# Optimization experiments

Measured on AMD Instinct MI355X. Metric: run time of the kernel, lower is better.

## Reference

```python
import jax, jax.numpy as jnp
import numpy as np

B, S, D, H = 2, 2048, 1024, 16
DK = D // H


def setup_inputs() -> dict:
    key = jax.random.key(0)
    ks = jax.random.split(key, 12)
    sc = 0.02
    inp = {
        'query': jax.random.normal(ks[0], (B, S, D), jnp.float32),
        'key': jax.random.normal(ks[1], (B, S, D), jnp.float32),
        'value': jax.random.normal(ks[2], (B, S, D), jnp.float32),
        # causal mask: positions with mask==0 are disallowed (matches masked_fill(mask==0, -inf))
        'mask': jnp.broadcast_to(jnp.tril(jnp.ones((S, S), jnp.int32)), (B, S, S)),
        'Wq': jax.random.normal(ks[3], (D, D), jnp.float32) * sc,
        'bq': jax.random.normal(ks[4], (D,), jnp.float32) * sc,
        'Wk': jax.random.normal(ks[5], (D, D), jnp.float32) * sc,
        'bk': jax.random.normal(ks[6], (D,), jnp.float32) * sc,
        'Wv': jax.random.normal(ks[7], (D, D), jnp.float32) * sc,
        'bv': jax.random.normal(ks[8], (D,), jnp.float32) * sc,
        'Wo': jax.random.normal(ks[9], (D, D), jnp.float32) * sc,
        'bo': jax.random.normal(ks[10], (D,), jnp.float32) * sc,
    }
    return inp


def reference(query, key, value, mask, Wq, bq, Wk, bk, Wv, bv, Wo, bo):
    # Linear projections (torch Linear: x @ W.T + b), split heads -> [B,H,S,DK]
    def proj(x, W, b):
        return (x @ W.T + b).reshape(B, S, H, DK).transpose(0, 2, 1, 3)

    q = proj(query, Wq, bq)
    k = proj(key, Wk, bk)
    v = proj(value, Wv, bv)

    scores = jnp.einsum('bhqd,bhkd->bhqk', q, k) / jnp.sqrt(jnp.float32(DK))
    # mask unsqueezed over head dim: [B,1,S,S]
    scores = jnp.where(mask[:, None, :, :] == 0, -jnp.inf, scores)
    p = jax.nn.softmax(scores, axis=-1)
    x = jnp.einsum('bhqk,bhkd->bhqd', p, v)  # [B,H,S,DK]
    x = x.transpose(0, 2, 1, 3).reshape(B, S, D)
    return x @ Wo.T + bo
```

## Files before the change

kernel.cpp:

```cpp
#include <hip/hip_runtime.h>
#include <hip/hip_bf16.h>
#include <math.h>

#define BATCH 2
#define SEQ 2048
#define DMODEL 1024
#define NHEAD 16
#define DHEAD 64
#define MTOT (BATCH*SEQ)

typedef __attribute__((ext_vector_type(8))) short bf16x8;
typedef __attribute__((ext_vector_type(4))) short short4v;
typedef __attribute__((ext_vector_type(4))) float f32x4;

static __device__ inline short f2bs(float x) {
    __hip_bfloat16 b = __float2bfloat16(x);
    return *reinterpret_cast<short*>(&b);
}

static __device__ __forceinline__ void gload16(const void* g, void* l) {
    __builtin_amdgcn_global_load_lds(
        (const __attribute__((address_space(1))) unsigned int*)g,
        (__attribute__((address_space(3))) unsigned int*)l,
        16, 0, 0);
}

struct ConvArgs {
    const float* src[7];
    unsigned short* dst[7];
    int nblk[7];
};

__global__ __launch_bounds__(256)
void convert_bf16_kernel(ConvArgs a)
{
    int b = blockIdx.x;
    int r = 0;
    while (b >= a.nblk[r]) { b -= a.nblk[r]; ++r; }
    const float* s = a.src[r];
    unsigned short* d = a.dst[r];
    const int base = b * 2048 + threadIdx.x * 8;
    const float4 f0 = *reinterpret_cast<const float4*>(&s[base]);
    const float4 f1 = *reinterpret_cast<const float4*>(&s[base + 4]);
    bf16x8 o;
    o[0] = f2bs(f0.x); o[1] = f2bs(f0.y); o[2] = f2bs(f0.z); o[3] = f2bs(f0.w);
    o[4] = f2bs(f1.x); o[5] = f2bs(f1.y); o[6] = f2bs(f1.z); o[7] = f2bs(f1.w);
    *reinterpret_cast<bf16x8*>(&d[base]) = o;
}

template<int SPLIT>
static __device__ __forceinline__
void gemm_core(const short* __restrict__ Xg, const short* __restrict__ Wg,
               const float* __restrict__ bias, void* __restrict__ outp,
               float scale, int m0, int n0)
{
    __shared__ short Xs[128 * 64];
    __shared__ short Wt[128 * 64];

    const int t    = threadIdx.x;
    const int lane = t & 63;
    const int w    = t >> 6;
    const int wm   = w >> 1, wn = w & 1;
    const int m_   = lane & 15, g = lane >> 4;

    const int sr  = t >> 1;
    const int sc0 = (t & 1) * 4;

    f32x4 acc[4][4] = {};
    bf16x8 xr[4], wr[4];

    auto ldtile = [&](int k0) {
        #pragma unroll
        for (int c = 0; c < 4; ++c) {
            xr[c] = *reinterpret_cast<const bf16x8*>(&Xg[(size_t)(m0 + sr) * DMODEL + k0 + (sc0 + c) * 8]);
            wr[c] = *reinterpret_cast<const bf16x8*>(&Wg[(size_t)(n0 + sr) * DMODEL + k0 + (sc0 + c) * 8]);
        }
    };
    auto sttile = [&]() {
        #pragma unroll
        for (int c = 0; c < 4; ++c) {
            const int byo = sr * 128 + (((sc0 + c) * 16) ^ ((sr & 7) << 4));
            *reinterpret_cast<bf16x8*>((char*)Xs + byo) = xr[c];
            *reinterpret_cast<bf16x8*>((char*)Wt + byo) = wr[c];
        }
    };

    ldtile(0);
    sttile();
    __syncthreads();

    for (int kt = 0; kt < DMODEL / 64; ++kt) {
        const bool more = (kt < DMODEL / 64 - 1);
        if (more) ldtile((kt + 1) * 64);

        bf16x8 af[4][2], bfr[4][2];
        #pragma unroll
        for (int mt = 0; mt < 4; ++mt) {
            const int row = wm * 64 + mt * 16 + m_;
            #pragma unroll
            for (int kc = 0; kc < 2; ++kc)
                af[mt][kc] = *reinterpret_cast<const bf16x8*>(
                    (char*)Xs + row * 128 + ((kc * 64 + g * 16) ^ ((row & 7) << 4)));
        }
        #pragma unroll
        for (int nt = 0; nt < 4; ++nt) {
            const int row = wn * 64 + nt * 16 + m_;
            #pragma unroll
            for (int kc = 0; kc < 2; ++kc)
                bfr[nt][kc] = *reinterpret_cast<const bf16x8*>(
                    (char*)Wt + row * 128 + ((kc * 64 + g * 16) ^ ((row & 7) << 4)));
        }

        __builtin_amdgcn_s_setprio(1);
        #pragma unroll
        for (int mt = 0; mt < 4; ++mt)
            #pragma unroll
            for (int nt = 0; nt < 4; ++nt)
                #pragma unroll
                for (int kc = 0; kc < 2; ++kc)
                    acc[mt][nt] = __builtin_amdgcn_mfma_f32_16x16x32_bf16(
                        af[mt][kc], bfr[nt][kc], acc[mt][nt], 0, 0, 0);
        __builtin_amdgcn_s_setprio(0);

        __syncthreads();
        if (more) sttile();
        __syncthreads();
    }

    float bv[4];
    #pragma unroll
    for (int nt = 0; nt < 4; ++nt) bv[nt] = bias[n0 + wn * 64 + nt * 16 + m_];

    #pragma unroll
    for (int mt = 0; mt < 4; ++mt) {
        #pragma unroll
        for (int r = 0; r < 4; ++r) {
            const int row = m0 + wm * 64 + mt * 16 + g * 4 + r;
            const int b = row >> 11;
            const int s = row & 2047;
            #pragma unroll
            for (int nt = 0; nt < 4; ++nt) {
                const int n = n0 + wn * 64 + nt * 16 + m_;
                const float c = (acc[mt][nt][r] + bv[nt]) * scale;
                if (SPLIT) {
                    const int h = n >> 6, dk = n & 63;
                    ((__hip_bfloat16*)outp)[(((size_t)(b * NHEAD + h)) * SEQ + s) * DHEAD + dk]
                        = __float2bfloat16(c);
                } else {
                    ((float*)outp)[(size_t)row * DMODEL + n] = c;
                }
            }
        }
    }
}

struct TrioArgs {
    const short* X[3];
    const short* W[3];
    const float* bias[3];
    __hip_bfloat16* out[3];
    float scale[3];
};

__global__ __launch_bounds__(256)
void gemm_qkv_kernel(TrioArgs a)
{
    const int bid = blockIdx.x;
    const int swz = (bid & 7) * 96 + (bid >> 3);
    const int which = swz >> 8;
    const int tile  = swz & 255;
    const int n0 = (tile & 7) * 128;
    const int m0 = (tile >> 3) * 128;
    gemm_core<1>(a.X[which], a.W[which], a.bias[which], a.out[which],
                 a.scale[which], m0, n0);
}

__global__ __launch_bounds__(256)
void gemm_out_kernel(const short* __restrict__ X, const short* __restrict__ W,
                     const float* __restrict__ bias, float* __restrict__ out)
{
    const int bid = blockIdx.x;
    const int swz = (bid & 7) * 32 + (bid >> 3);
    const int n0 = (swz & 7) * 128;
    const int m0 = (swz >> 3) * 128;
    gemm_core<0>(X, W, bias, out, 1.0f, m0, n0);
}

__global__ __launch_bounds__(512, 4)
void attn_mfma_kernel(const __hip_bfloat16* __restrict__ Q,
                      const __hip_bfloat16* __restrict__ K,
                      const __hip_bfloat16* __restrict__ V,
                      __hip_bfloat16* __restrict__ ctx)
{
    __shared__ short Ks[2][64 * 64];
    __shared__ short Vts[2][64 * 64];
    __shared__ short Ps[8 * 16 * 72];

    const int t    = threadIdx.x;
    const int lane = t & 63;
    const int w    = t >> 6;
    const int wq   = w & 3;
    const int side = w >> 2;
    const int m    = lane & 15;
    const int g    = lane >> 4;

    const int bid = blockIdx.x;
    const int swz = (bid & 7) * 64 + (bid >> 3);
    const int bh  = swz >> 4;
    const int pr  = swz & 15;
    const int qtA = pr, qtB = 31 - pr;
    const int myqt = side ? qtB : qtA;
    const int q0   = myqt * 64;

    const __hip_bfloat16* Qb = Q + (size_t)bh * SEQ * DHEAD;
    const __hip_bfloat16* Kb = K + (size_t)bh * SEQ * DHEAD;
    const __hip_bfloat16* Vb = V + (size_t)bh * SEQ * DHEAD;

    const int sKrb = 16 * (w & 3);
    const int krl  = lane >> 3;
    const int kcs  = (lane & 7) ^ krl;
    const int vk   = t & 63;
    const int vd0  = ((t >> 6) & 3) * 16;

    bf16x8 vreg0, vreg1;
    auto stageK = [&](int k0s, int buf) {
        #pragma unroll
        for (int c2 = 0; c2 < 2; ++c2) {
            const int rb = sKrb + 8 * c2;
            gload16(Kb + (size_t)(k0s + rb + krl) * DHEAD + kcs * 8,
                    &Ks[buf][rb * 64]);
        }
    };
    auto loadV = [&](int k0s) {
        vreg0 = *reinterpret_cast<const bf16x8*>(&Vb[(size_t)(k0s + vk) * DHEAD + vd0]);
        vreg1 = *reinterpret_cast<const bf16x8*>(&Vb[(size_t)(k0s + vk) * DHEAD + vd0 + 8]);
    };
    auto writeV = [&](int buf) {
        #pragma unroll
        for (int j = 0; j < 8; ++j) {
            const int d = vd0 + j;
            *reinterpret_cast<short*>((char*)Vts[buf] +
                (((d * 128) + vk * 2) ^ ((d & 7) << 4))) = vreg0[j];
        }
        #pragma unroll
        for (int j = 0; j < 8; ++j) {
            const int d = vd0 + 8 + j;
            *reinterpret_cast<short*>((char*)Vts[buf] +
                (((d * 128) + vk * 2) ^ ((d & 7) << 4))) = vreg1[j];
        }
    };

    bf16x8 qf[2];
    #pragma unroll
    for (int c = 0; c < 2; ++c)
        qf[c] = *reinterpret_cast<const bf16x8*>(
            &Qb[(size_t)(q0 + 16 * wq + m) * DHEAD + c * 32 + 8 * g]);

    f32x4 o[4] = {};
    float mr = -INFINITY, lr = 0.0f;

    short* Pw = Ps + w * 16 * 72;

    if (t < 256) { stageK(0, 0); loadV(0); writeV(0); }
    __syncthreads();

    int cur = 0;
    for (int kt = 0; kt <= qtB; ++kt) {
        const bool more = (kt < qtB);
        if (t < 256 && more) {
            stageK((kt + 1) * 64, cur ^ 1);
            loadV((kt + 1) * 64);
        }

        if (kt <= myqt) {
            f32x4 s[4] = {};
            __builtin_amdgcn_s_setprio(1);
            #pragma unroll
            for (int ct = 0; ct < 4; ++ct) {
                const int krow = ct * 16 + m;
                #pragma unroll
                for (int c = 0; c < 2; ++c) {
                    const bf16x8 kf = *reinterpret_cast<const bf16x8*>((char*)Ks[cur] +
                        (((krow * 128) + c * 64 + 16 * g) ^ ((krow & 7) << 4)));
                    s[ct] = __builtin_amdgcn_mfma_f32_16x16x32_bf16(kf, qf[c], s[ct], 0, 0, 0);
                }
            }
            __builtin_amdgcn_s_setprio(0);

            if (kt == myqt) {
                const int qr = 16 * wq + m;
                #pragma unroll
                for (int ct = 0; ct < 4; ++ct)
                    #pragma unroll
                    for (int r = 0; r < 4; ++r)
                        if (ct * 16 + 4 * g + r > qr) s[ct][r] = -INFINITY;
            }

            float pmax = fmaxf(fmaxf(s[0][0], s[0][1]), fmaxf(s[0][2], s[0][3]));
            pmax = fmaxf(fmaxf(pmax, s[1][0]), s[1][1]);
            pmax = fmaxf(fmaxf(pmax, s[1][2]), s[1][3]);
            pmax = fmaxf(fmaxf(pmax, s[2][0]), s[2][1]);
            pmax = fmaxf(fmaxf(pmax, s[2][2]), s[2][3]);
            pmax = fmaxf(fmaxf(pmax, s[3][0]), s[3][1]);
            pmax = fmaxf(fmaxf(pmax, s[3][2]), s[3][3]);
            pmax = fmaxf(pmax, __shfl_xor(pmax, 16, 64));
            pmax = fmaxf(pmax, __shfl_xor(pmax, 32, 64));

            if (!__all(pmax <= mr + 8.0f)) {
                const float mnew = fmaxf(mr, pmax);
                const float scl  = __builtin_amdgcn_exp2f(mr - mnew);
                mr = mnew;
                lr *= scl;
                #pragma unroll
                for (int dt = 0; dt < 4; ++dt)
                    #pragma unroll
                    for (int r = 0; r < 4; ++r)
                        o[dt][r] *= scl;
            }

            float psum = 0.0f;
            #pragma unroll
            for (int ct = 0; ct < 4; ++ct) {
                #pragma unroll
                for (int r = 0; r < 4; ++r) {
                    s[ct][r] = __builtin_amdgcn_exp2f(s[ct][r] - mr);
                    psum += s[ct][r];
                }
            }
            psum += __shfl_xor(psum, 16, 64);
            psum += __shfl_xor(psum, 32, 64);
            lr += psum;

            #pragma unroll
            for (int ct = 0; ct < 4; ++ct) {
                short4v p4;
                p4[0] = f2bs(s[ct][0]); p4[1] = f2bs(s[ct][1]);
                p4[2] = f2bs(s[ct][2]); p4[3] = f2bs(s[ct][3]);
                *reinterpret_cast<short4v*>(&Pw[m * 72 + ct * 16 + 4 * g]) = p4;
            }

            bf16x8 pf[2];
            #pragma unroll
            for (int c = 0; c < 2; ++c)
                pf[c] = *reinterpret_cast<const bf16x8*>(&Pw[m * 72 + c * 32 + 8 * g]);

            __builtin_amdgcn_s_setprio(1);
            #pragma unroll
            for (int dt = 0; dt < 4; ++dt) {
                const int vrow = dt * 16 + m;
                #pragma unroll
                for (int c = 0; c < 2; ++c) {
                    const bf16x8 vf = *reinterpret_cast<const bf16x8*>((char*)Vts[cur] +
                        (((vrow * 128) + c * 64 + 16 * g) ^ ((vrow & 7) << 4)));
                    o[dt] = __builtin_amdgcn_mfma_f32_16x16x32_bf16(vf, pf[c], o[dt], 0, 0, 0);
                }
            }
            __builtin_amdgcn_s_setprio(0);
        }

        if (t < 256 && more) writeV(cur ^ 1);
        __syncthreads();
        cur ^= 1;
    }

    const int b = bh >> 4;
    const int h = bh & 15;
    const float inv = 1.0f / lr;
    const int row = q0 + 16 * wq + m;
    short* dst = (short*)&ctx[((size_t)(b * SEQ) + row) * DMODEL + h * DHEAD];
    #pragma unroll
    for (int dt = 0; dt < 4; ++dt) {
        short4v p4;
        p4[0] = f2bs(o[dt][0] * inv); p4[1] = f2bs(o[dt][1] * inv);
        p4[2] = f2bs(o[dt][2] * inv); p4[3] = f2bs(o[dt][3] * inv);
        *reinterpret_cast<short4v*>(dst + dt * 16 + 4 * g) = p4;
    }
}

extern "C" void kernel_launch(void* const* d_in, const int* in_sizes, int n_in,
                              void* d_out, int out_size, void* d_ws, size_t ws_size,
                              hipStream_t stream)
{
    const float* query = (const float*)d_in[0];
    const float* key   = (const float*)d_in[1];
    const float* value = (const float*)d_in[2];
    const float* Wq = (const float*)d_in[4];
    const float* bq = (const float*)d_in[5];
    const float* Wk = (const float*)d_in[6];
    const float* bk = (const float*)d_in[7];
    const float* Wv = (const float*)d_in[8];
    const float* bv = (const float*)d_in[9];
    const float* Wo = (const float*)d_in[10];
    const float* bo = (const float*)d_in[11];
    float* out = (float*)d_out;

    char* ws = (char*)d_ws;
    const size_t MB = 1024 * 1024;
    unsigned short* xq  = (unsigned short*)(ws + 0 * MB);
    unsigned short* xk  = (unsigned short*)(ws + 8 * MB);
    unsigned short* xv  = (unsigned short*)(ws + 16 * MB);
    unsigned short* wqb = (unsigned short*)(ws + 24 * MB);
    unsigned short* wkb = (unsigned short*)(ws + 26 * MB);
    unsigned short* wvb = (unsigned short*)(ws + 28 * MB);
    unsigned short* wob = (unsigned short*)(ws + 30 * MB);
    __hip_bfloat16* qb  = (__hip_bfloat16*)(ws + 32 * MB);
    __hip_bfloat16* kb  = (__hip_bfloat16*)(ws + 40 * MB);
    __hip_bfloat16* vb  = (__hip_bfloat16*)(ws + 48 * MB);
    __hip_bfloat16* ctx = (__hip_bfloat16*)(ws + 56 * MB);

    ConvArgs ca;
    ca.src[0] = query; ca.dst[0] = xq;  ca.nblk[0] = 2048;
    ca.src[1] = key;   ca.dst[1] = xk;  ca.nblk[1] = 2048;
    ca.src[2] = value; ca.dst[2] = xv;  ca.nblk[2] = 2048;
    ca.src[3] = Wq;    ca.dst[3] = wqb; ca.nblk[3] = 512;
    ca.src[4] = Wk;    ca.dst[4] = wkb; ca.nblk[4] = 512;
    ca.src[5] = Wv;    ca.dst[5] = wvb; ca.nblk[5] = 512;
    ca.src[6] = Wo;    ca.dst[6] = wob; ca.nblk[6] = 512;
    convert_bf16_kernel<<<dim3(8192), dim3(256), 0, stream>>>(ca);

    TrioArgs ta;
    ta.X[0] = (const short*)xq; ta.W[0] = (const short*)wqb; ta.bias[0] = bq;
    ta.out[0] = qb; ta.scale[0] = 0.125f * 1.44269504f;
    ta.X[1] = (const short*)xk; ta.W[1] = (const short*)wkb; ta.bias[1] = bk;
    ta.out[1] = kb; ta.scale[1] = 1.0f;
    ta.X[2] = (const short*)xv; ta.W[2] = (const short*)wvb; ta.bias[2] = bv;
    ta.out[2] = vb; ta.scale[2] = 1.0f;
    gemm_qkv_kernel<<<dim3(768), dim3(256), 0, stream>>>(ta);

    attn_mfma_kernel<<<dim3(512), dim3(512), 0, stream>>>(qb, kb, vb, ctx);

    gemm_out_kernel<<<dim3(256), dim3(256), 0, stream>>>(
        (const short*)ctx, (const short*)wob, bo, out);
}
```

Before: 116.4 us.

## Balance causal attention work across wave halves with split-KV merge for long tile

Each half of the block (4 waves per side) now gets its own K/V stream, and the work is split evenly. The short-tile side finishes its tile and then takes part of the long tile's KV range, so both sides run 17 iterations instead of one side idling while the other does up to 32. The partial softmax states for the long tile are merged through shared memory at the end. K staging moves from direct global-to-LDS loads to register loads plus LDS writes done by all 512 threads, and each iteration now has two barriers.

```diff
diff --git a/kernel.cpp b/kernel.cpp
--- a/kernel.cpp
+++ b/kernel.cpp
@@ -16,13 +16,6 @@
 static __device__ inline short f2bs(float x) {
     __hip_bfloat16 b = __float2bfloat16(x);
     return *reinterpret_cast<short*>(&b);
-}
-
-static __device__ __forceinline__ void gload16(const void* g, void* l) {
-    __builtin_amdgcn_global_load_lds(
-        (const __attribute__((address_space(1))) unsigned int*)g,
-        (__attribute__((address_space(3))) unsigned int*)l,
-        16, 0, 0);
 }
 
 struct ConvArgs {
@@ -192,9 +185,7 @@
                       const __hip_bfloat16* __restrict__ V,
                       __hip_bfloat16* __restrict__ ctx)
 {
-    __shared__ short Ks[2][64 * 64];
-    __shared__ short Vts[2][64 * 64];
-    __shared__ short Ps[8 * 16 * 72];
+    __shared__ short smem[25600];
 
     const int t    = threadIdx.x;
     const int lane = t & 63;
@@ -204,90 +195,103 @@
     const int m    = lane & 15;
     const int g    = lane >> 4;
 
+    short* Ksd = smem + side * 4096;
+    short* Vtd = smem + 8192 + side * 4096;
+    short* Pw  = smem + 16384 + w * (16 * 72);
+
     const int bid = blockIdx.x;
     const int swz = (bid & 7) * 64 + (bid >> 3);
     const int bh  = swz >> 4;
     const int pr  = swz & 15;
     const int qtA = pr, qtB = 31 - pr;
-    const int myqt = side ? qtB : qtA;
-    const int q0   = myqt * 64;
+    const int Na  = qtA + 1;
+    const int Nb  = qtB + 1;
+    const int c   = (Nb - Na) >> 1;
+    const int njobs = side ? (Nb - c) : (Na + c);
 
     const __hip_bfloat16* Qb = Q + (size_t)bh * SEQ * DHEAD;
     const __hip_bfloat16* Kb = K + (size_t)bh * SEQ * DHEAD;
     const __hip_bfloat16* Vb = V + (size_t)bh * SEQ * DHEAD;
 
-    const int sKrb = 16 * (w & 3);
-    const int krl  = lane >> 3;
-    const int kcs  = (lane & 7) ^ krl;
-    const int vk   = t & 63;
-    const int vd0  = ((t >> 6) & 3) * 16;
-
-    bf16x8 vreg0, vreg1;
-    auto stageK = [&](int k0s, int buf) {
-        #pragma unroll
-        for (int c2 = 0; c2 < 2; ++c2) {
-            const int rb = sKrb + 8 * c2;
-            gload16(Kb + (size_t)(k0s + rb + krl) * DHEAD + kcs * 8,
-                    &Ks[buf][rb * 64]);
-        }
+    const int q0A = qtA * 64, q0B = qtB * 64;
+
+    const int u    = t & 255;
+    const int krow = u >> 2;
+    const int kch  = u & 3;
+    const int vk   = u & 63;
+    const int vd0  = (u >> 6) * 16;
+
+    bf16x8 kreg[2], vreg[2];
+    auto kvOf = [&](int j) -> int {
+        return side ? (c + j) : ((j < Na) ? j : (j - Na));
     };
-    auto loadV = [&](int k0s) {
-        vreg0 = *reinterpret_cast<const bf16x8*>(&Vb[(size_t)(k0s + vk) * DHEAD + vd0]);
-        vreg1 = *reinterpret_cast<const bf16x8*>(&Vb[(size_t)(k0s + vk) * DHEAD + vd0 + 8]);
+    auto loadKV = [&](int j) {
+        const int k0 = kvOf(j) * 64;
+        kreg[0] = *reinterpret_cast<const bf16x8*>(&Kb[(size_t)(k0 + krow) * DHEAD + kch * 8]);
+        kreg[1] = *reinterpret_cast<const bf16x8*>(&Kb[(size_t)(k0 + krow) * DHEAD + (kch + 4) * 8]);
+        vreg[0] = *reinterpret_cast<const bf16x8*>(&Vb[(size_t)(k0 + vk) * DHEAD + vd0]);
+        vreg[1] = *reinterpret_cast<const bf16x8*>(&Vb[(size_t)(k0 + vk) * DHEAD + vd0 + 8]);
     };
-    auto writeV = [&](int buf) {
+    auto writeKV = [&]() {
+        *reinterpret_cast<bf16x8*>((char*)Ksd +
+            (krow * 128 + ((kch * 16) ^ ((krow & 7) << 4)))) = kreg[0];
+        *reinterpret_cast<bf16x8*>((char*)Ksd +
+            (krow * 128 + (((kch + 4) * 16) ^ ((krow & 7) << 4)))) = kreg[1];
         #pragma unroll
         for (int j = 0; j < 8; ++j) {
             const int d = vd0 + j;
-            *reinterpret_cast<short*>((char*)Vts[buf] +
-                (((d * 128) + vk * 2) ^ ((d & 7) << 4))) = vreg0[j];
+            *reinterpret_cast<short*>((char*)Vtd +
+                (((d * 128) + vk * 2) ^ ((d & 7) << 4))) = vreg[0][j];
         }
         #pragma unroll
         for (int j = 0; j < 8; ++j) {
             const int d = vd0 + 8 + j;
-            *reinterpret_cast<short*>((char*)Vts[buf] +
-                (((d * 128) + vk * 2) ^ ((d & 7) << 4))) = vreg1[j];
+            *reinterpret_cast<short*>((char*)Vtd +
+                (((d * 128) + vk * 2) ^ ((d & 7) << 4))) = vreg[1][j];
         }
     };
 
-    bf16x8 qf[2];
+    const int myq0 = side ? q0B : q0A;
+    bf16x8 qfP[2], qfS[2];
     #pragma unroll
-    for (int c = 0; c < 2; ++c)
-        qf[c] = *reinterpret_cast<const bf16x8*>(
-            &Qb[(size_t)(q0 + 16 * wq + m) * DHEAD + c * 32 + 8 * g]);
+    for (int c2 = 0; c2 < 2; ++c2) {
+        qfP[c2] = *reinterpret_cast<const bf16x8*>(
+            &Qb[(size_t)(myq0 + 16 * wq + m) * DHEAD + c2 * 32 + 8 * g]);
+        qfS[c2] = side ? qfP[c2] : *reinterpret_cast<const bf16x8*>(
+            &Qb[(size_t)(q0B + 16 * wq + m) * DHEAD + c2 * 32 + 8 * g]);
+    }
 
     f32x4 o[4] = {};
     float mr = -INFINITY, lr = 0.0f;
 
-    short* Pw = Ps + w * 16 * 72;
-
-    if (t < 256) { stageK(0, 0); loadV(0); writeV(0); }
+    loadKV(0);
+    writeKV();
     __syncthreads();
 
-    int cur = 0;
-    for (int kt = 0; kt <= qtB; ++kt) {
-        const bool more = (kt < qtB);
-        if (t < 256 && more) {
-            stageK((kt + 1) * 64, cur ^ 1);
-            loadV((kt + 1) * 64);
-        }
-
-        if (kt <= myqt) {
+    for (int j = 0; j < 17; ++j) {
+        const bool haveNext = (j + 1 < njobs);
+        if (haveNext) loadKV(j + 1);
+
+        if (j < njobs) {
+            const bool inA = (!side) && (j < Na);
+            const bool diag = side ? (j == 16) : (inA && j == Na - 1);
+
             f32x4 s[4] = {};
             __builtin_amdgcn_s_setprio(1);
             #pragma unroll
             for (int ct = 0; ct < 4; ++ct) {
-                const int krow = ct * 16 + m;
-                #pragma unroll
-                for (int c = 0; c < 2; ++c) {
-                    const bf16x8 kf = *reinterpret_cast<const bf16x8*>((char*)Ks[cur] +
-                        (((krow * 128) + c * 64 + 16 * g) ^ ((krow & 7) << 4)));
-                    s[ct] = __builtin_amdgcn_mfma_f32_16x16x32_bf16(kf, qf[c], s[ct], 0, 0, 0);
+                const int kr = ct * 16 + m;
+                #pragma unroll
+                for (int c2 = 0; c2 < 2; ++c2) {
+                    const bf16x8 kf = *reinterpret_cast<const bf16x8*>((char*)Ksd +
+                        ((kr * 128) + ((c2 * 64 + 16 * g) ^ ((kr & 7) << 4))));
+                    const bf16x8 qv = inA ? qfP[c2] : (side ? qfP[c2] : qfS[c2]);
+                    s[ct] = __builtin_amdgcn_mfma_f32_16x16x32_bf16(kf, qv, s[ct], 0, 0, 0);
                 }
             }
             __builtin_amdgcn_s_setprio(0);
 
-            if (kt == myqt) {
+            if (diag) {
                 const int qr = 16 * wq + m;
                 #pragma unroll
                 for (int ct = 0; ct < 4; ++ct)
@@ -338,42 +342,85 @@
                 p4[2] = f2bs(s[ct][2]); p4[3] = f2bs(s[ct][3]);
                 *reinterpret_cast<short4v*>(&Pw[m * 72 + ct * 16 + 4 * g]) = p4;
             }
-
             bf16x8 pf[2];
             #pragma unroll
-            for (int c = 0; c < 2; ++c)
-                pf[c] = *reinterpret_cast<const bf16x8*>(&Pw[m * 72 + c * 32 + 8 * g]);
+            for (int c2 = 0; c2 < 2; ++c2)
+                pf[c2] = *reinterpret_cast<const bf16x8*>(&Pw[m * 72 + c2 * 32 + 8 * g]);
 
             __builtin_amdgcn_s_setprio(1);
             #pragma unroll
             for (int dt = 0; dt < 4; ++dt) {
-                const int vrow = dt * 16 + m;
-                #pragma unroll
-                for (int c = 0; c < 2; ++c) {
-                    const bf16x8 vf = *reinterpret_cast<const bf16x8*>((char*)Vts[cur] +
-                        (((vrow * 128) + c * 64 + 16 * g) ^ ((vrow & 7) << 4)));
-                    o[dt] = __builtin_amdgcn_mfma_f32_16x16x32_bf16(vf, pf[c], o[dt], 0, 0, 0);
+                const int vr = dt * 16 + m;
+                #pragma unroll
+                for (int c2 = 0; c2 < 2; ++c2) {
+                    const bf16x8 vf = *reinterpret_cast<const bf16x8*>((char*)Vtd +
+                        (((vr * 128) + c2 * 64 + 16 * g) ^ ((vr & 7) << 4)));
+                    o[dt] = __builtin_amdgcn_mfma_f32_16x16x32_bf16(vf, pf[c2], o[dt], 0, 0, 0);
                 }
             }
             __builtin_amdgcn_s_setprio(0);
-        }
-
-        if (t < 256 && more) writeV(cur ^ 1);
+
+            if (!side && j == Na - 1) {
+                const int b = bh >> 4, h = bh & 15;
+                const float inv = 1.0f / lr;
+                const int row = q0A + 16 * wq + m;
+                short* dst = (short*)&ctx[((size_t)(b * SEQ) + row) * DMODEL + h * DHEAD];
+                #pragma unroll
+                for (int dt = 0; dt < 4; ++dt) {
+                    short4v p4;
+                    p4[0] = f2bs(o[dt][0] * inv); p4[1] = f2bs(o[dt][1] * inv);
+                    p4[2] = f2bs(o[dt][2] * inv); p4[3] = f2bs(o[dt][3] * inv);
+                    *reinterpret_cast<short4v*>(dst + dt * 16 + 4 * g) = p4;
+                }
+                mr = -INFINITY; lr = 0.0f;
+                #pragma unroll
+                for (int dt = 0; dt < 4; ++dt)
+                    #pragma unroll
+                    for (int r = 0; r < 4; ++r)
+                        o[dt][r] = 0.0f;
+            }
+        }
+
         __syncthreads();
-        cur ^= 1;
-    }
-
-    const int b = bh >> 4;
-    const int h = bh & 15;
-    const float inv = 1.0f / lr;
-    const int row = q0 + 16 * wq + m;
-    short* dst = (short*)&ctx[((size_t)(b * SEQ) + row) * DMODEL + h * DHEAD];
-    #pragma unroll
-    for (int dt = 0; dt < 4; ++dt) {
-        short4v p4;
-        p4[0] = f2bs(o[dt][0] * inv); p4[1] = f2bs(o[dt][1] * inv);
-        p4[2] = f2bs(o[dt][2] * inv); p4[3] = f2bs(o[dt][3] * inv);
-        *reinterpret_cast<short4v*>(dst + dt * 16 + 4 * g) = p4;
+        if (haveNext) writeKV();
+        __syncthreads();
+    }
+
+    float* o0area = (float*)smem;
+    float* mlarea = (float*)(smem + 8192);
+    if (!side) {
+        #pragma unroll
+        for (int dt = 0; dt < 4; ++dt)
+            #pragma unroll
+            for (int r = 0; r < 4; ++r)
+                o0area[wq * 1024 + m * 64 + ((dt * 16 + 4 * g + r) ^ ((m & 7) << 2))] = o[dt][r];
+        if (g == 0) {
+            mlarea[wq * 32 + m]      = mr;
+            mlarea[wq * 32 + 16 + m] = lr;
+        }
+    }
+    __syncthreads();
+    if (side) {
+        const float m0 = mlarea[wq * 32 + m];
+        const float l0 = mlarea[wq * 32 + 16 + m];
+        const float mm = fmaxf(m0, mr);
+        const float s0 = __builtin_amdgcn_exp2f(m0 - mm);
+        const float s1 = __builtin_amdgcn_exp2f(mr - mm);
+        const float inv = 1.0f / (l0 * s0 + lr * s1);
+
+        const int b = bh >> 4, h = bh & 15;
+        const int row = q0B + 16 * wq + m;
+        short* dst = (short*)&ctx[((size_t)(b * SEQ) + row) * DMODEL + h * DHEAD];
+        #pragma unroll
+        for (int dt = 0; dt < 4; ++dt) {
+            short4v p4;
+            #pragma unroll
+            for (int r = 0; r < 4; ++r) {
+                const float o0 = o0area[wq * 1024 + m * 64 + ((dt * 16 + 4 * g + r) ^ ((m & 7) << 2))];
+                p4[r] = f2bs((o0 * s0 + o[dt][r] * s1) * inv);
+            }
+            *reinterpret_cast<short4v*>(dst + dt * 16 + 4 * g) = p4;
+        }
     }
 }
 
```

After: 121.4 us. +4.3%, slower.

## Double-buffer GEMM tiles with direct global-to-LDS loads and BK=32

Applied to the files above, without the earlier changes.

Replaces the register-staged global→LDS copy in the projection GEMM with global_load_lds direct copies into a double-buffered shared tile, halving the K-tile to 32 so both buffers fit in the same LDS footprint. This removes the VGPR staging registers and one __syncthreads per iteration, letting the next tile's load overlap the current MFMAs. In exchange there are twice as many K iterations, each with its own barrier and fewer MFMAs per barrier. The XOR swizzle is changed to match the new 64-byte row layout.

```diff
diff --git a/kernel.cpp b/kernel.cpp
--- a/kernel.cpp
+++ b/kernel.cpp
@@ -54,8 +54,8 @@
                const float* __restrict__ bias, void* __restrict__ outp,
                float scale, int m0, int n0)
 {
-    __shared__ short Xs[128 * 64];
-    __shared__ short Wt[128 * 64];
+    __shared__ short Xs[2][128 * 32];
+    __shared__ short Wt[2][128 * 32];
 
     const int t    = threadIdx.x;
     const int lane = t & 63;
@@ -63,52 +63,42 @@
     const int wm   = w >> 1, wn = w & 1;
     const int m_   = lane & 15, g = lane >> 4;
 
-    const int sr  = t >> 1;
-    const int sc0 = (t & 1) * 4;
+    const int srl = lane >> 2;
+    const int scs = (lane & 3) ^ ((lane >> 3) & 3);
+
+    auto stage = [&](int k0, int buf) {
+        #pragma unroll
+        for (int c = 0; c < 2; ++c) {
+            const int rowb = 32 * w + 16 * c;
+            gload16(Xg + (size_t)(m0 + rowb + srl) * DMODEL + k0 + scs * 8,
+                    &Xs[buf][rowb * 32]);
+            gload16(Wg + (size_t)(n0 + rowb + srl) * DMODEL + k0 + scs * 8,
+                    &Wt[buf][rowb * 32]);
+        }
+    };
 
     f32x4 acc[4][4] = {};
-    bf16x8 xr[4], wr[4];
-
-    auto ldtile = [&](int k0) {
-        #pragma unroll
-        for (int c = 0; c < 4; ++c) {
-            xr[c] = *reinterpret_cast<const bf16x8*>(&Xg[(size_t)(m0 + sr) * DMODEL + k0 + (sc0 + c) * 8]);
-            wr[c] = *reinterpret_cast<const bf16x8*>(&Wg[(size_t)(n0 + sr) * DMODEL + k0 + (sc0 + c) * 8]);
-        }
-    };
-    auto sttile = [&]() {
-        #pragma unroll
-        for (int c = 0; c < 4; ++c) {
-            const int byo = sr * 128 + (((sc0 + c) * 16) ^ ((sr & 7) << 4));
-            *reinterpret_cast<bf16x8*>((char*)Xs + byo) = xr[c];
-            *reinterpret_cast<bf16x8*>((char*)Wt + byo) = wr[c];
-        }
-    };
-
-    ldtile(0);
-    sttile();
+
+    stage(0, 0);
     __syncthreads();
 
-    for (int kt = 0; kt < DMODEL / 64; ++kt) {
-        const bool more = (kt < DMODEL / 64 - 1);
-        if (more) ldtile((kt + 1) * 64);
-
-        bf16x8 af[4][2], bfr[4][2];
+    int buf = 0;
+    for (int kt = 0; kt < DMODEL / 32; ++kt) {
+        if (kt < DMODEL / 32 - 1) stage((kt + 1) * 32, buf ^ 1);
+
+        bf16x8 af[4], bfr[4];
+        const int cp = (g ^ ((m_ >> 1) & 3)) << 4;
         #pragma unroll
         for (int mt = 0; mt < 4; ++mt) {
             const int row = wm * 64 + mt * 16 + m_;
-            #pragma unroll
-            for (int kc = 0; kc < 2; ++kc)
-                af[mt][kc] = *reinterpret_cast<const bf16x8*>(
-                    (char*)Xs + row * 128 + ((kc * 64 + g * 16) ^ ((row & 7) << 4)));
+            af[mt] = *reinterpret_cast<const bf16x8*>(
+                (char*)Xs[buf] + row * 64 + cp);
         }
         #pragma unroll
         for (int nt = 0; nt < 4; ++nt) {
             const int row = wn * 64 + nt * 16 + m_;
-            #pragma unroll
-            for (int kc = 0; kc < 2; ++kc)
-                bfr[nt][kc] = *reinterpret_cast<const bf16x8*>(
-                    (char*)Wt + row * 128 + ((kc * 64 + g * 16) ^ ((row & 7) << 4)));
+            bfr[nt] = *reinterpret_cast<const bf16x8*>(
+                (char*)Wt[buf] + row * 64 + cp);
         }
 
         __builtin_amdgcn_s_setprio(1);
@@ -116,15 +106,12 @@
         for (int mt = 0; mt < 4; ++mt)
             #pragma unroll
             for (int nt = 0; nt < 4; ++nt)
-                #pragma unroll
-                for (int kc = 0; kc < 2; ++kc)
-                    acc[mt][nt] = __builtin_amdgcn_mfma_f32_16x16x32_bf16(
-                        af[mt][kc], bfr[nt][kc], acc[mt][nt], 0, 0, 0);
+                acc[mt][nt] = __builtin_amdgcn_mfma_f32_16x16x32_bf16(
+                    af[mt], bfr[nt], acc[mt][nt], 0, 0, 0);
         __builtin_amdgcn_s_setprio(0);
 
         __syncthreads();
-        if (more) sttile();
-        __syncthreads();
+        buf ^= 1;
     }
 
     float bv[4];
```

After: 119.1 us. +2.3%, slower.
